# Optimization experiments

Hardware: AMD Instinct MI355X
Metric: run time of the kernel (lower is better)

The kernel has to match this reference:

```python
import jax, jax.numpy as jnp
import numpy as np

CONTEXT = 5
PAD = CONTEXT // 2
EPS = 1e-12  # torch F.normalize eps


def _conv2d(x, w, b):
    # x: [B,Cin,H,W], w: [Cout,Cin,3,3], SAME padding (pad=1)
    y = jax.lax.conv_general_dilated(
        x, w, window_strides=(1, 1), padding='SAME',
        dimension_numbers=('NCHW', 'OIHW', 'NCHW'))
    return y + b[None, :, None, None]


def _self_similarity(fn):
    # fn: L2-normalized features [B,C,H,W] -> cost volume [B,25,H,W]
    b, c, h, w = fn.shape
    fp = jnp.pad(fn, ((0, 0), (0, 0), (PAD, PAD), (PAD, PAD)))
    # channel index = col*CONTEXT + row, matching the torch loop order
    planes = [
        (fp[:, :, r:h + r, cc:w + cc] * fn).sum(axis=1)
        for cc in range(CONTEXT) for r in range(CONTEXT)
    ]
    return jnp.stack(planes, axis=1)


def setup_inputs() -> dict:
    key = jax.random.key(0)
    ks = jax.random.split(key, 5)
    B, C, H, W = 8, 512, 96, 96
    OC = 128
    return {
        'feature': jax.random.normal(ks[0], (B, C, H, W), dtype=jnp.float32),
        'w0': jax.random.normal(ks[1], (2 * OC, CONTEXT * CONTEXT, 3, 3), dtype=jnp.float32) * 0.05,
        'b0': jax.random.normal(ks[2], (2 * OC,), dtype=jnp.float32) * 0.01,
        'w1': jax.random.normal(ks[3], (OC, 2 * OC, 3, 3), dtype=jnp.float32) * 0.05,
        'b1': jax.random.normal(ks[4], (OC,), dtype=jnp.float32) * 0.01,
    }


def reference(feature, w0, b0, w1, b1):
    # F.normalize(p=2, dim=1): divide by channel L2 norm clamped to eps
    norm = jnp.sqrt((feature * feature).sum(axis=1, keepdims=True))
    fn = feature / jnp.maximum(norm, EPS)
    ss = _self_similarity(fn)                 # [B,25,H,W]
    ss1 = jax.nn.relu(_conv2d(ss, w0, b0))    # [B,256,H,W]
    ss2 = jax.nn.relu(_conv2d(ss1, w1, b1))   # [B,128,H,W]
    return jnp.concatenate((ss, ss1, ss2), axis=1)  # [B,409,H,W]
```

## Files before the change

### kernel.cpp

```cpp
#include <hip/hip_runtime.h>

#define FEAT_C 512
#define Hh 96
#define Ww 96
#define HW (Hh*Ww)
#define NB 8
#define OUTC 409

typedef __attribute__((ext_vector_type(8))) short short8;
typedef __attribute__((ext_vector_type(4))) short short4v;
typedef __attribute__((ext_vector_type(4))) float f32x4;
typedef __fp16 h2 __attribute__((ext_vector_type(2)));
typedef __fp16 h8 __attribute__((ext_vector_type(8)));

typedef __attribute__((address_space(1))) const unsigned int gu32;
typedef __attribute__((address_space(3))) unsigned int lu32;

__device__ inline ushort f2bf(float x) {
    unsigned u = __float_as_uint(x);
    u += 0x7fffu + ((u >> 16) & 1u);
    return (ushort)(u >> 16);
}

#if __has_builtin(__builtin_amdgcn_fdot2)
__device__ inline float FDOT2(h2 a, h2 b, float c) {
    return __builtin_amdgcn_fdot2(a, b, c, false);
}
#else
__device__ inline float FDOT2(h2 a, h2 b, float c) {
    return c + (float)a[0] * (float)b[0] + (float)a[1] * (float)b[1];
}
#endif

__device__ inline h2 pair(h8 v, int i) {
    switch (i) {
        case 0: return __builtin_shufflevector(v, v, 0, 1);
        case 1: return __builtin_shufflevector(v, v, 2, 3);
        case 2: return __builtin_shufflevector(v, v, 4, 5);
        default: return __builtin_shufflevector(v, v, 6, 7);
    }
}

#define PKPX 32
__global__ __launch_bounds__(256) void kpack(const float* __restrict__ f,
                                             ushort* __restrict__ fnorm) {
    __shared__ ushort tr[PKPX * 512];
    __shared__ float ssqp[8][PKPX];
    __shared__ float sinvs[PKPX];
    int tid = threadIdx.x;
    int g = tid >> 5, pl = tid & 31;
    int b = blockIdx.y;
    int p0 = blockIdx.x * PKPX;
    const float* fb = f + (size_t)b * FEAT_C * HW + p0 + pl;

    float ssq = 0.f;
#pragma unroll
    for (int q = 0; q < 8; ++q) {
        int u = g * 8 + q;
        float v[8];
#pragma unroll
        for (int j = 0; j < 8; ++j)
            v[j] = fb[(size_t)(u * 8 + j) * HW];
        h2 a0 = __builtin_amdgcn_cvt_pkrtz(v[0], v[1]);
        h2 a1 = __builtin_amdgcn_cvt_pkrtz(v[2], v[3]);
        h2 a2 = __builtin_amdgcn_cvt_pkrtz(v[4], v[5]);
        h2 a3 = __builtin_amdgcn_cvt_pkrtz(v[6], v[7]);
        ssq = FDOT2(a0, a0, ssq); ssq = FDOT2(a1, a1, ssq);
        ssq = FDOT2(a2, a2, ssq); ssq = FDOT2(a3, a3, ssq);
        h8 hv;
        hv[0] = a0[0]; hv[1] = a0[1]; hv[2] = a1[0]; hv[3] = a1[1];
        hv[4] = a2[0]; hv[5] = a2[1]; hv[6] = a3[0]; hv[7] = a3[1];
        int up = u ^ (pl & 7);
        *(h8*)&tr[pl * 512 + up * 8] = hv;
    }
    ssqp[g][pl] = ssq;
    __syncthreads();
    if (tid < PKPX) {
        float s = 0.f;
#pragma unroll
        for (int gg = 0; gg < 8; ++gg) s += ssqp[gg][tid];
        sinvs[tid] = 1.0f / fmaxf(sqrtf(s), 1e-12f);
    }
    __syncthreads();

    size_t ob = ((size_t)b * HW + p0) * 512;
#pragma unroll
    for (int i = 0; i < 8; ++i) {
        int t = tid + i * 256;
        int r = t >> 6, k = t & 63;
        h8 hv = *(const h8*)&tr[r * 512 + ((k ^ (r & 7)) * 8)];
        float s = sinvs[r];
        h2 o0 = __builtin_amdgcn_cvt_pkrtz((float)hv[0] * s, (float)hv[1] * s);
        h2 o1 = __builtin_amdgcn_cvt_pkrtz((float)hv[2] * s, (float)hv[3] * s);
        h2 o2 = __builtin_amdgcn_cvt_pkrtz((float)hv[4] * s, (float)hv[5] * s);
        h2 o3 = __builtin_amdgcn_cvt_pkrtz((float)hv[6] * s, (float)hv[7] * s);
        h8 ov;
        ov[0] = o0[0]; ov[1] = o0[1]; ov[2] = o1[0]; ov[3] = o1[1];
        ov[4] = o2[0]; ov[5] = o2[1]; ov[6] = o3[0]; ov[7] = o3[1];
        *(h8*)&fnorm[ob + (size_t)r * 512 + k * 8] = ov;
    }
}

#define SS_NPX 240
__global__ __launch_bounds__(256) void kss4(const ushort* __restrict__ fnorm,
                                            float* __restrict__ out,
                                            ushort* __restrict__ sspk0) {
    __shared__ ushort tile[2][SS_NPX * 32];
    int tid = threadIdx.x;
    int w = tid >> 6, lane = tid & 63;
    int s = lane >> 4, q = lane & 15;
    int x0 = blockIdx.x * 16, y0 = blockIdx.y * 8, b = blockIdx.z;

    size_t t_src[4];
    int t_dst[4];
    bool t_ok[4];
#pragma unroll
    for (int k = 0; k < 4; ++k) {
        int task = tid + k * 256;
        t_ok[k] = false; t_src[k] = 0; t_dst[k] = -1;
        if (task < 960) {
            int px = task >> 2, u = task & 3;
            int hr = px / 20, hc = px % 20;
            int gy = y0 + hr - 2, gx = x0 + hc - 2;
            t_dst[k] = px * 32 + ((u ^ ((px >> 1) & 3)) * 8);
            if (gy >= 0 && gy < Hh && gx >= 0 && gx < Ww) {
                t_ok[k] = true;
                t_src[k] = ((size_t)b * HW + (size_t)gy * Ww + gx) * 512 + u * 8;
            }
        }
    }

    float acc0[25], acc1[25];
#pragma unroll
    for (int o = 0; o < 25; ++o) { acc0[o] = 0.f; acc1[o] = 0.f; }

    auto stage = [&](int chunk, int nbuf) {
        short8 v[4];
#pragma unroll
        for (int k = 0; k < 4; ++k) {
            v[k] = (short8)0;
            if (t_ok[k]) v[k] = *(const short8*)(fnorm + t_src[k] + chunk * 32);
        }
#pragma unroll
        for (int k = 0; k < 4; ++k)
            if (t_dst[k] >= 0)
                *(short8*)&tile[nbuf][t_dst[k]] = v[k];
    };

    auto compute = [&](int kb) {
        const ushort* tb = tile[kb];
        auto rd = [&](int px) -> h8 {
            return *(const h8*)&tb[px * 32 + ((s ^ ((px >> 1) & 3)) * 8)];
        };
        int pc0 = (2 * w + 2) * 20 + q + 2;
        h8 c0 = rd(pc0);
        h8 c1 = rd(pc0 + 20);
#pragma unroll
        for (int dxc = 0; dxc < 5; ++dxc) {
#pragma unroll
            for (int dyr = 0; dyr < 6; ++dyr) {
                int pn = (2 * w + dyr) * 20 + q + dxc;
                h8 nv = rd(pn);
                if (dyr < 5) {
                    float a = acc0[dxc * 5 + dyr];
                    a = FDOT2(pair(nv, 0), pair(c0, 0), a);
                    a = FDOT2(pair(nv, 1), pair(c0, 1), a);
                    a = FDOT2(pair(nv, 2), pair(c0, 2), a);
                    a = FDOT2(pair(nv, 3), pair(c0, 3), a);
                    acc0[dxc * 5 + dyr] = a;
                }
                if (dyr > 0) {
                    float a = acc1[dxc * 5 + dyr - 1];
                    a = FDOT2(pair(nv, 0), pair(c1, 0), a);
                    a = FDOT2(pair(nv, 1), pair(c1, 1), a);
                    a = FDOT2(pair(nv, 2), pair(c1, 2), a);
                    a = FDOT2(pair(nv, 3), pair(c1, 3), a);
                    acc1[dxc * 5 + dyr - 1] = a;
                }
            }
        }
    };

    stage(0, 0);
    __syncthreads();
    for (int c = 0; c < 16; ++c) {
        if (c < 15) stage(c + 1, (c + 1) & 1);
        compute(c & 1);
        __syncthreads();
    }

#pragma unroll
    for (int o = 0; o < 25; ++o) {
        float v0 = acc0[o];
        v0 += __shfl_xor(v0, 16);
        v0 += __shfl_xor(v0, 32);
        acc0[o] = v0;
        float v1 = acc1[o];
        v1 += __shfl_xor(v1, 16);
        v1 += __shfl_xor(v1, 32);
        acc1[o] = v1;
    }
    if (s == 0) {
        int gy0 = y0 + 2 * w, gx = x0 + q;
        size_t pix0 = (size_t)b * HW + (size_t)gy0 * Ww + gx;
        size_t ob0 = (size_t)b * OUTC * HW + (size_t)gy0 * Ww + gx;
#pragma unroll
        for (int o = 0; o < 25; ++o) {
            out[ob0 + (size_t)o * HW] = acc0[o];
            out[ob0 + (size_t)o * HW + Ww] = acc1[o];
        }
        ushort pk0[32], pk1[32];
#pragma unroll
        for (int o = 0; o < 25; ++o) { pk0[o] = f2bf(acc0[o]); pk1[o] = f2bf(acc1[o]); }
#pragma unroll
        for (int o = 25; o < 32; ++o) { pk0[o] = 0; pk1[o] = 0; }
#pragma unroll
        for (int u = 0; u < 4; ++u) {
            *(short8*)&sspk0[pix0 * 32 + u * 8] = *(short8*)&pk0[u * 8];
            *(short8*)&sspk0[(pix0 + Ww) * 32 + u * 8] = *(short8*)&pk1[u * 8];
        }
    }
}

__global__ __launch_bounds__(256) void kwpack0(const float* __restrict__ w0,
                                               ushort* __restrict__ wpk0) {
    int i = blockIdx.x * 256 + threadIdx.x;
    if (i >= 9 * 256 * 32) return;
    int t = i >> 13, oc = (i >> 5) & 255;
    int s = (i >> 3) & 3, ii = i & 7;
    int u = s ^ ((oc >> 1) & 3);
    int ic = u * 8 + ii;
    wpk0[i] = (ic < 25) ? f2bf(w0[(size_t)oc * 225 + ic * 9 + t]) : (ushort)0;
}

__global__ __launch_bounds__(256) void kwpack1(const float* __restrict__ w1,
                                               ushort* __restrict__ wpk1) {
    int i = blockIdx.x * 256 + threadIdx.x;
    if (i >= 8 * 9 * 128 * 32) return;
    int ct = i >> 12;
    int c = ct / 9, t = ct % 9;
    int oc = (i >> 5) & 127;
    int s = (i >> 3) & 3, ii = i & 7;
    int u = s ^ ((oc >> 1) & 3);
    int ic = c * 32 + u * 8 + ii;
    wpk1[i] = f2bf(w1[((size_t)oc * 256 + ic) * 9 + t]);
}

#define C1NPX 180
__global__ __launch_bounds__(512, 2) void kconv1m(const ushort* __restrict__ sspk0,
                                                  const ushort* __restrict__ wpk0,
                                                  const float* __restrict__ b0,
                                                  float* __restrict__ outp,
                                                  ushort* __restrict__ sspk) {
    __shared__ ushort wlds[2][8192];
    __shared__ ushort plds[C1NPX * 32];
    int tid = threadIdx.x;
    int lane = tid & 63, wid = tid >> 6;
    int wM = wid >> 1, wN = wid & 1;
    int l15 = lane & 15, l4 = lane >> 4;
    int x0 = blockIdx.x * 16, y0 = blockIdx.y * 8, b = blockIdx.z;

    auto wstage = [&](int t, int buf) {
        const ushort* src = wpk0 + (size_t)t * 8192 + wid * 1024 + lane * 8;
        ushort* dst = &wlds[buf][wid * 1024];
#pragma unroll
        for (int i = 0; i < 2; ++i)
            __builtin_amdgcn_global_load_lds((gu32*)(src + i * 512),
                                             (lu32*)(dst + i * 512), 16, 0, 0);
    };

    wstage(0, 0);

    {
        short8 v[2]; int dst[2];
#pragma unroll
        for (int k = 0; k < 2; ++k) {
            int task = tid + k * 512;
            v[k] = (short8)0; dst[k] = -1;
            if (task < 720) {
                int px = task >> 2, u = task & 3;
                int iy = px / 18, ix = px % 18;
                int gy = y0 + iy - 1, gx = x0 + ix - 1;
                dst[k] = px * 32 + (u ^ ((px >> 1) & 3)) * 8;
                if (gy >= 0 && gy < Hh && gx >= 0 && gx < Ww)
                    v[k] = *(const short8*)(sspk0 +
                            ((size_t)b * HW + (size_t)gy * Ww + gx) * 32 + u * 8);
            }
        }
#pragma unroll
        for (int k = 0; k < 2; ++k)
            if (dst[k] >= 0) *(short8*)&plds[dst[k]] = v[k];
    }
    __syncthreads();

    f32x4 acc[4][4];
#pragma unroll
    for (int mi = 0; mi < 4; ++mi)
#pragma unroll
        for (int ni = 0; ni < 4; ++ni)
            acc[mi][ni] = (f32x4)0.f;

    int wslot = l4 ^ ((l15 >> 1) & 3);
    for (int t = 0; t < 9; ++t) {
        if (t < 8) wstage(t + 1, (t + 1) & 1);
        int ky = t / 3, kx = t % 3;
        const ushort* wbase = wlds[t & 1];
        short8 a[4], bv[4];
#pragma unroll
        for (int mi = 0; mi < 4; ++mi) {
            int row = wM * 64 + mi * 16 + l15;
            a[mi] = *(const short8*)&wbase[row * 32 + wslot * 8];
        }
#pragma unroll
        for (int ni = 0; ni < 4; ++ni) {
            int ipx = (wN * 4 + ni + ky) * 18 + l15 + kx;
            bv[ni] = *(const short8*)&plds[ipx * 32
                    + ((l4 ^ ((ipx >> 1) & 3)) * 8)];
        }
#pragma unroll
        for (int mi = 0; mi < 4; ++mi)
#pragma unroll
            for (int ni = 0; ni < 4; ++ni)
                acc[mi][ni] = __builtin_amdgcn_mfma_f32_16x16x32_bf16(
                    a[mi], bv[ni], acc[mi][ni], 0, 0, 0);
        __syncthreads();
    }

    size_t ob = (size_t)b * OUTC * HW + (size_t)25 * HW;
    size_t pb = (size_t)b * HW;
#pragma unroll
    for (int mi = 0; mi < 4; ++mi)
#pragma unroll
        for (int ni = 0; ni < 4; ++ni) {
            int gy = y0 + wN * 4 + ni, gx = x0 + l15;
            int oc_b = wM * 64 + mi * 16 + l4 * 4;
            short4v hv;
#pragma unroll
            for (int r = 0; r < 4; ++r) {
                float v = fmaxf(acc[mi][ni][r] + b0[oc_b + r], 0.f);
                outp[ob + (size_t)(oc_b + r) * HW + (size_t)gy * Ww + gx] = v;
                hv[r] = (short)f2bf(v);
            }
            *(short4v*)&sspk[(pb + (size_t)gy * Ww + gx) * 256 + oc_b] = hv;
        }
}

#define NPX2 180
#define WGRP 12288
__global__ __launch_bounds__(256, 2) void kconv2n(const ushort* __restrict__ sspk,
                                                  const ushort* __restrict__ wpk,
                                                  const float* __restrict__ b1,
                                                  float* __restrict__ outp) {
    __shared__ ushort wlds[2][WGRP];
    __shared__ ushort plds[2][NPX2 * 32];
    int tid = threadIdx.x;
    int lane = tid & 63, wid = tid >> 6;
    int wM = wid >> 1, wN = wid & 1;
    int l15 = lane & 15, l4 = lane >> 4;
    int x0 = blockIdx.x * 16, y0 = blockIdx.y * 8, b = blockIdx.z;

    f32x4 acc[4][4];
#pragma unroll
    for (int mi = 0; mi < 4; ++mi)
#pragma unroll
        for (int ni = 0; ni < 4; ++ni)
            acc[mi][ni] = (f32x4)0.f;

    size_t t_src[3];
    int t_dst[3];
    bool t_ok[3];
#pragma unroll
    for (int k = 0; k < 3; ++k) {
        int task = tid + k * 256;
        t_ok[k] = false; t_src[k] = 0; t_dst[k] = -1;
        if (task < 720) {
            int px = task >> 2, u = task & 3;
            int iy = px / 18, ix = px % 18;
            int gy = y0 + iy - 1, gx = x0 + ix - 1;
            t_dst[k] = px * 32 + (u ^ ((px >> 1) & 3)) * 8;
            if (gy >= 0 && gy < Hh && gx >= 0 && gx < Ww) {
                t_ok[k] = true;
                t_src[k] = ((size_t)b * HW + (size_t)gy * Ww + gx) * 256 + u * 8;
            }
        }
    }

    auto stage_load = [&](int c, short8* v) {
#pragma unroll
        for (int k = 0; k < 3; ++k) {
            v[k] = (short8)0;
            if (t_ok[k])
                v[k] = *(const short8*)(sspk + t_src[k] + c * 32);
        }
    };
    auto stage_write = [&](int nbuf, short8* v) {
#pragma unroll
        for (int k = 0; k < 3; ++k)
            if (t_dst[k] >= 0)
                *(short8*)&plds[nbuf][t_dst[k]] = v[k];
    };

    auto wstage = [&](int gi, int buf) {
        const ushort* src = wpk + (size_t)gi * WGRP + wid * 3072 + lane * 8;
        ushort* dst = &wlds[buf][wid * 3072];
#pragma unroll
        for (int i = 0; i < 6; ++i)
            __builtin_amdgcn_global_load_lds((gu32*)(src + i * 512),
                                             (lu32*)(dst + i * 512), 16, 0, 0);
    };

    int wslot = l4 ^ ((l15 >> 1) & 3);
    auto compute = [&](int wb, int pb_, int ky) {
        const ushort* wbase = wlds[wb];
        const ushort* lbase = plds[pb_];
#pragma unroll
        for (int kx = 0; kx < 3; ++kx) {
            short8 a[4], bv[4];
#pragma unroll
            for (int mi = 0; mi < 4; ++mi) {
                int row = wM * 64 + mi * 16 + l15;
                a[mi] = *(const short8*)&wbase[(kx * 128 + row) * 32 + wslot * 8];
            }
#pragma unroll
            for (int ni = 0; ni < 4; ++ni) {
                int oy = wN * 4 + ni;
                int ipx = (oy + ky) * 18 + l15 + kx;
                bv[ni] = *(const short8*)&lbase[ipx * 32
                        + ((l4 ^ ((ipx >> 1) & 3)) * 8)];
            }
#pragma unroll
            for (int mi = 0; mi < 4; ++mi)
#pragma unroll
                for (int ni = 0; ni < 4; ++ni)
                    acc[mi][ni] = __builtin_amdgcn_mfma_f32_16x16x32_bf16(
                        a[mi], bv[ni], acc[mi][ni], 0, 0, 0);
        }
    };

    wstage(0, 0);
    {
        short8 sv[3];
        stage_load(0, sv);
        stage_write(0, sv);
    }
    __syncthreads();

    for (int c = 0; c < 8; ++c) {
        int gi = c * 3;
        short8 nv[3];
        wstage(gi + 1, (gi + 1) & 1);
        if (c < 7) stage_load(c + 1, nv);
        compute(gi & 1, c & 1, 0);
        __syncthreads();
        wstage(gi + 2, (gi + 2) & 1);
        compute((gi + 1) & 1, c & 1, 1);
        __syncthreads();
        if (gi + 3 < 24) wstage(gi + 3, (gi + 3) & 1);
        if (c < 7) stage_write((c + 1) & 1, nv);
        compute((gi + 2) & 1, c & 1, 2);
        __syncthreads();
    }

    size_t ob = (size_t)b * OUTC * HW + (size_t)281 * HW;
#pragma unroll
    for (int mi = 0; mi < 4; ++mi)
#pragma unroll
        for (int ni = 0; ni < 4; ++ni) {
            int gy = y0 + wN * 4 + ni, gx = x0 + l15;
#pragma unroll
            for (int r = 0; r < 4; ++r) {
                int oc = wM * 64 + mi * 16 + l4 * 4 + r;
                float v = acc[mi][ni][r] + b1[oc];
                outp[ob + (size_t)oc * HW + (size_t)gy * Ww + gx] = fmaxf(v, 0.f);
            }
        }
}

extern "C" void kernel_launch(void* const* d_in, const int* in_sizes, int n_in,
                              void* d_out, int out_size, void* d_ws, size_t ws_size,
                              hipStream_t stream) {
    const float* feat = (const float*)d_in[0];
    const float* w0   = (const float*)d_in[1];
    const float* b0   = (const float*)d_in[2];
    const float* w1   = (const float*)d_in[3];
    const float* b1   = (const float*)d_in[4];
    float* out = (float*)d_out;

    ushort* wpk0  = (ushort*)d_ws;
    ushort* wpk1  = (ushort*)((char*)d_ws + 147456);
    ushort* sspk  = (ushort*)((char*)d_ws + 147456 + 589824);
    ushort* fnorm = (ushort*)((char*)d_ws + 147456 + 589824 + 37748736);
    ushort* sspk0 = (ushort*)((char*)d_ws + 147456 + 589824 + 37748736
                              + 75497472);

    hipLaunchKernelGGL(kwpack0, dim3(288),  dim3(256), 0, stream, w0, wpk0);
    hipLaunchKernelGGL(kwpack1, dim3(1152), dim3(256), 0, stream, w1, wpk1);
    hipLaunchKernelGGL(kpack,   dim3(HW / PKPX, NB), dim3(256), 0, stream, feat, fnorm);
    hipLaunchKernelGGL(kss4,    dim3(6, 12, NB), dim3(256), 0, stream, fnorm, out, sspk0);
    hipLaunchKernelGGL(kconv1m, dim3(6, 12, NB), dim3(512), 0, stream, sspk0, wpk0, b0, out, sspk);
    hipLaunchKernelGGL(kconv2n, dim3(6, 12, NB), dim3(256), 0, stream, sspk, wpk1, b1, out);
}
```

Measured before the change: 207.0 us.

## Stage conv2 pixel tiles via direct global-to-LDS loads with vmcnt-based pipelining

In the second conv kernel, the pixel-tile staging that went through registers (global load, then LDS store) is replaced by global_load_lds DMA into a pre-swizzled LDS layout, with a zero-pad buffer standing in for out-of-bounds pixels. Full __syncthreads are replaced by explicit vmcnt/lgkmcnt waits plus raw s_barrier so the weight and pixel prefetches can stay in flight across compute phases; the first conv kernel gets the same barrier treatment. This is meant to remove register staging and over-conservative waits, at the cost of relying on hand-counted vmcnt values being exactly right.

```diff
diff --git a/kernel.cpp b/kernel.cpp
--- a/kernel.cpp
+++ b/kernel.cpp
@@ -15,6 +15,11 @@
 
 typedef __attribute__((address_space(1))) const unsigned int gu32;
 typedef __attribute__((address_space(3))) unsigned int lu32;
+
+#define VMCNT(N) do { asm volatile("s_waitcnt vmcnt(" #N ")" ::: "memory"); \
+                      __builtin_amdgcn_sched_barrier(0); } while (0)
+#define LGKM0()  do { asm volatile("s_waitcnt lgkmcnt(0)" ::: "memory"); \
+                      __builtin_amdgcn_sched_barrier(0); } while (0)
 
 __device__ inline ushort f2bf(float x) {
     unsigned u = __float_as_uint(x);
@@ -234,7 +239,9 @@
 }
 
 __global__ __launch_bounds__(256) void kwpack1(const float* __restrict__ w1,
-                                               ushort* __restrict__ wpk1) {
+                                               ushort* __restrict__ wpk1,
+                                               ushort* __restrict__ zpad) {
+    if (blockIdx.x == 0 && threadIdx.x < 32) zpad[threadIdx.x] = 0;
     int i = blockIdx.x * 256 + threadIdx.x;
     if (i >= 8 * 9 * 128 * 32) return;
     int ct = i >> 12;
@@ -291,7 +298,9 @@
         for (int k = 0; k < 2; ++k)
             if (dst[k] >= 0) *(short8*)&plds[dst[k]] = v[k];
     }
-    __syncthreads();
+    LGKM0();
+    VMCNT(0);
+    __builtin_amdgcn_s_barrier();
 
     f32x4 acc[4][4];
 #pragma unroll
@@ -302,7 +311,9 @@
 
     int wslot = l4 ^ ((l15 >> 1) & 3);
     for (int t = 0; t < 9; ++t) {
-        if (t < 8) wstage(t + 1, (t + 1) & 1);
+        if (t < 8) { wstage(t + 1, (t + 1) & 1); VMCNT(2); }
+        else       { VMCNT(0); }
+        __builtin_amdgcn_s_barrier();
         int ky = t / 3, kx = t % 3;
         const ushort* wbase = wlds[t & 1];
         short8 a[4], bv[4];
@@ -323,7 +334,8 @@
             for (int ni = 0; ni < 4; ++ni)
                 acc[mi][ni] = __builtin_amdgcn_mfma_f32_16x16x32_bf16(
                     a[mi], bv[ni], acc[mi][ni], 0, 0, 0);
-        __syncthreads();
+        LGKM0();
+        __builtin_amdgcn_s_barrier();
     }
 
     size_t ob = (size_t)b * OUTC * HW + (size_t)25 * HW;
@@ -350,9 +362,10 @@
 __global__ __launch_bounds__(256, 2) void kconv2n(const ushort* __restrict__ sspk,
                                                   const ushort* __restrict__ wpk,
                                                   const float* __restrict__ b1,
+                                                  const ushort* __restrict__ zpad,
                                                   float* __restrict__ outp) {
     __shared__ ushort wlds[2][WGRP];
-    __shared__ ushort plds[2][NPX2 * 32];
+    __shared__ ushort plds[2][6144];
     int tid = threadIdx.x;
     int lane = tid & 63, wid = tid >> 6;
     int wM = wid >> 1, wN = wid & 1;
@@ -366,40 +379,28 @@
         for (int ni = 0; ni < 4; ++ni)
             acc[mi][ni] = (f32x4)0.f;
 
-    size_t t_src[3];
-    int t_dst[3];
-    bool t_ok[3];
+    const ushort* p_src[3];
+    int p_ok[3];
 #pragma unroll
     for (int k = 0; k < 3; ++k) {
         int task = tid + k * 256;
-        t_ok[k] = false; t_src[k] = 0; t_dst[k] = -1;
-        if (task < 720) {
-            int px = task >> 2, u = task & 3;
-            int iy = px / 18, ix = px % 18;
-            int gy = y0 + iy - 1, gx = x0 + ix - 1;
-            t_dst[k] = px * 32 + (u ^ ((px >> 1) & 3)) * 8;
-            if (gy >= 0 && gy < Hh && gx >= 0 && gx < Ww) {
-                t_ok[k] = true;
-                t_src[k] = ((size_t)b * HW + (size_t)gy * Ww + gx) * 256 + u * 8;
-            }
-        }
-    }
-
-    auto stage_load = [&](int c, short8* v) {
-#pragma unroll
-        for (int k = 0; k < 3; ++k) {
-            v[k] = (short8)0;
-            if (t_ok[k])
-                v[k] = *(const short8*)(sspk + t_src[k] + c * 32);
-        }
+        int px = task >> 2, slot = task & 3;
+        int u = slot ^ ((px >> 1) & 3);
+        int iy = px / 18, ix = px % 18;
+        int gy = y0 + iy - 1, gx = x0 + ix - 1;
+        bool ok = (px < NPX2) && gy >= 0 && gy < Hh && gx >= 0 && gx < Ww;
+        p_ok[k] = ok ? 1 : 0;
+        p_src[k] = ok ? (sspk + ((size_t)b * HW + (size_t)gy * Ww + gx) * 256
+                         + u * 8)
+                      : zpad;
+    }
+    auto pstage = [&](int c, int buf) {
+#pragma unroll
+        for (int k = 0; k < 3; ++k)
+            __builtin_amdgcn_global_load_lds(
+                (gu32*)(p_src[k] + (p_ok[k] ? c * 32 : 0)),
+                (lu32*)&plds[buf][(k * 256 + wid * 64) * 8], 16, 0, 0);
     };
-    auto stage_write = [&](int nbuf, short8* v) {
-#pragma unroll
-        for (int k = 0; k < 3; ++k)
-            if (t_dst[k] >= 0)
-                *(short8*)&plds[nbuf][t_dst[k]] = v[k];
-    };
-
     auto wstage = [&](int gi, int buf) {
         const ushort* src = wpk + (size_t)gi * WGRP + wid * 3072 + lane * 8;
         ushort* dst = &wlds[buf][wid * 3072];
@@ -435,30 +436,30 @@
                     acc[mi][ni] = __builtin_amdgcn_mfma_f32_16x16x32_bf16(
                         a[mi], bv[ni], acc[mi][ni], 0, 0, 0);
         }
+        LGKM0();
     };
 
+    pstage(0, 0);
     wstage(0, 0);
-    {
-        short8 sv[3];
-        stage_load(0, sv);
-        stage_write(0, sv);
-    }
-    __syncthreads();
 
     for (int c = 0; c < 8; ++c) {
-        int gi = c * 3;
-        short8 nv[3];
-        wstage(gi + 1, (gi + 1) & 1);
-        if (c < 7) stage_load(c + 1, nv);
-        compute(gi & 1, c & 1, 0);
-        __syncthreads();
-        wstage(gi + 2, (gi + 2) & 1);
-        compute((gi + 1) & 1, c & 1, 1);
-        __syncthreads();
-        if (gi + 3 < 24) wstage(gi + 3, (gi + 3) & 1);
-        if (c < 7) stage_write((c + 1) & 1, nv);
-        compute((gi + 2) & 1, c & 1, 2);
-        __syncthreads();
+        int wb = c & 1;
+        wstage(3 * c + 1, wb ^ 1);
+        VMCNT(6);
+        __builtin_amdgcn_s_barrier();
+        compute(wb, wb, 0);
+        __builtin_amdgcn_s_barrier();
+        wstage(3 * c + 2, wb);
+        if (c < 7) { pstage(c + 1, wb ^ 1); VMCNT(9); }
+        else       { VMCNT(6); }
+        __builtin_amdgcn_s_barrier();
+        compute(wb ^ 1, wb, 1);
+        __builtin_amdgcn_s_barrier();
+        if (c < 7) { wstage(3 * c + 3, wb ^ 1); VMCNT(9); }
+        else       { VMCNT(0); }
+        __builtin_amdgcn_s_barrier();
+        compute(wb, wb, 2);
+        __builtin_amdgcn_s_barrier();
     }
 
     size_t ob = (size_t)b * OUTC * HW + (size_t)281 * HW;
@@ -492,11 +493,13 @@
     ushort* fnorm = (ushort*)((char*)d_ws + 147456 + 589824 + 37748736);
     ushort* sspk0 = (ushort*)((char*)d_ws + 147456 + 589824 + 37748736
                               + 75497472);
+    ushort* zpad  = (ushort*)((char*)d_ws + 147456 + 589824 + 37748736
+                              + 75497472 + 4718592);
 
     hipLaunchKernelGGL(kwpack0, dim3(288),  dim3(256), 0, stream, w0, wpk0);
-    hipLaunchKernelGGL(kwpack1, dim3(1152), dim3(256), 0, stream, w1, wpk1);
+    hipLaunchKernelGGL(kwpack1, dim3(1152), dim3(256), 0, stream, w1, wpk1, zpad);
     hipLaunchKernelGGL(kpack,   dim3(HW / PKPX, NB), dim3(256), 0, stream, feat, fnorm);
     hipLaunchKernelGGL(kss4,    dim3(6, 12, NB), dim3(256), 0, stream, fnorm, out, sspk0);
     hipLaunchKernelGGL(kconv1m, dim3(6, 12, NB), dim3(512), 0, stream, sspk0, wpk0, b0, out, sspk);
-    hipLaunchKernelGGL(kconv2n, dim3(6, 12, NB), dim3(256), 0, stream, sspk, wpk1, b1, out);
-}
+    hipLaunchKernelGGL(kconv2n, dim3(6, 12, NB), dim3(256), 0, stream, sspk, wpk1, b1, zpad, out);
+}
```

Result: no change. 209.7 us (+1.3%).
